# Kernel tuning notes

Measured on AMD Instinct MI355X. Metric: run time of the kernel, lower is better.

The kernel has to match this reference:

```python
import jax, jax.numpy as jnp
import numpy as np

N = 500000
E = 500000
F = 128
BN_EPS = 1e-3


def setup_inputs() -> dict:
    key = jax.random.key(0)
    ks = jax.random.split(key, 8)
    return {
        "x": jax.random.normal(ks[0], (N, F), dtype=jnp.float32),
        "pairs_prev": jax.random.randint(ks[1], (E, 2), 0, N, dtype=jnp.int64),
        "pairs_next": jax.random.randint(ks[2], (E, 2), 0, N, dtype=jnp.int64),
        "w_next": jax.random.normal(ks[3], (F, F), dtype=jnp.float32),
        "w_prev": jax.random.normal(ks[4], (F, F), dtype=jnp.float32),
        "b": jnp.zeros((1, F), dtype=jnp.float32),
        "bn_gamma": jnp.ones((F,), dtype=jnp.float32),
        "bn_beta": jnp.zeros((F,), dtype=jnp.float32),
        "gru_kernel": jax.random.normal(ks[5], (F, 3 * F), dtype=jnp.float32) * 0.1,
        "gru_rec_kernel": jax.random.normal(ks[6], (F, 3 * F), dtype=jnp.float32) * 0.1,
        "gru_bias": jax.random.normal(ks[7], (2, 3 * F), dtype=jnp.float32) * 0.1,
    }


def _gru(x, h, kernel, rec_kernel, bias, hidden):
    matrix_x = x @ kernel + bias[0]            # (N, 3H)
    x_z, x_r, x_h = jnp.split(matrix_x, 3, axis=-1)
    matrix_inner = h @ rec_kernel + bias[1]    # (N, 3H)
    rec_z, rec_r, rec_h = jnp.split(matrix_inner, 3, axis=-1)
    z = jax.nn.sigmoid(x_z + rec_z)
    r = jax.nn.sigmoid(x_r + rec_r)
    h_cand = jnp.tanh(x_h + r * rec_h)
    return z * h + (1.0 - z) * h_cand


def reference(x, pairs_prev, pairs_next, w_next, w_prev, b,
              bn_gamma, bn_beta, gru_kernel, gru_rec_kernel, gru_bias):
    num_nodes = x.shape[0]
    # gather source-node features, scatter-add onto target nodes
    prev_sumx = jax.ops.segment_sum(x[pairs_prev[:, 1]], pairs_prev[:, 0],
                                    num_segments=num_nodes)
    next_sumx = jax.ops.segment_sum(x[pairs_next[:, 1]], pairs_next[:, 0],
                                    num_segments=num_nodes)
    aggre = next_sumx @ w_next + prev_sumx @ w_prev + b
    aggre = aggre + x  # multiply=None -> residual skip
    # BatchNorm1d (training mode): batch mean / biased variance over nodes
    a = jax.nn.relu(aggre)
    mean = jnp.mean(a, axis=0)
    var = jnp.mean((a - mean) ** 2, axis=0)
    a = (a - mean) * jax.lax.rsqrt(var + BN_EPS) * bn_gamma + bn_beta
    return _gru(a, x, gru_kernel, gru_rec_kernel, gru_bias, x.shape[1])
```

## Files before the change

### kernel.cpp

```cpp
#include <hip/hip_runtime.h>
#include <hip/hip_bf16.h>

#define N_NODES 500000
#define E_EDGES 500000
#define FDIM 128
#define BN_EPS 1e-3f
#define OFFS 500001

#define WS_BUCKETS 0
#define WS_SCALESHIFT 16384
#define WS_PW 16640
#define WS_PW2 65792
#define WS_XBF 82176

#define SO_CNT 0
#define SO_OFF 1000000
#define SO_PART 2100000
#define SO_CUR 2200000
#define SO_SRC 3200000

typedef __attribute__((ext_vector_type(4))) float v4f;
typedef __attribute__((ext_vector_type(8))) __bf16 v8bf;

__device__ __forceinline__ unsigned f2bf_u(float f) {
  unsigned u = __float_as_uint(f);
  return ((u + 0x7FFF + ((u >> 16) & 1)) >> 16) & 0xFFFF;
}
__device__ __forceinline__ unsigned f2bf2(float a, float b) {
  return f2bf_u(a) | (f2bf_u(b) << 16);
}
__device__ __forceinline__ float bf2f(unsigned short u) {
  return __uint_as_float((unsigned)u << 16);
}
__device__ __forceinline__ float fast_sigmoid(float x) {
  float e = __expf(-x);
  return __builtin_amdgcn_rcpf(1.f + e);
}
__device__ __forceinline__ float fast_tanh(float x) {
  x = fminf(fmaxf(x, -15.f), 15.f);
  float e = __expf(2.f * x);
  return (e - 1.f) * __builtin_amdgcn_rcpf(e + 1.f);
}

__global__ __launch_bounds__(256) void repack_gru(
    const float* __restrict__ gk, const float* __restrict__ rk,
    unsigned short* __restrict__ pw) {
  int idx = blockIdx.x * 256 + threadIdx.x;
  int side = idx / 49152;
  int rem = idx % 49152;
  int gate = rem >> 14;
  int rr = rem & 16383;
  int c = rr >> 7, k = rr & 127;
  const float* src = side ? rk : gk;
  float v = src[k * 384 + gate * 128 + c];
  int w = c >> 5, nb = (c >> 4) & 1, l15 = c & 15;
  int ks = k >> 5, lg = (k >> 3) & 3, j = k & 7;
  int lane = lg * 16 + l15;
  int e = w * 24576 + ks * 6144 + nb * 3072 + gate * 1024 + side * 512 + lane * 8 + j;
  pw[e] = (unsigned short)f2bf_u(v);
}

__global__ __launch_bounds__(256) void repack_w(
    const float* __restrict__ w_next, const float* __restrict__ w_prev,
    unsigned short* __restrict__ pw2) {
  int idx = blockIdx.x * 256 + threadIdx.x;
  int side = idx >> 14;
  int rr = idx & 16383;
  int c = rr >> 7, k = rr & 127;
  const float* src = side ? w_prev : w_next;
  float v = src[k * 128 + c];
  int nh = c >> 6, nb = (c >> 4) & 3, l15 = c & 15;
  int ks = k >> 5, lg = (k >> 3) & 3, j = k & 7;
  int lane = lg * 16 + l15;
  int e = nh * 16384 + ks * 4096 + nb * 1024 + side * 512 + lane * 8 + j;
  pw2[e] = (unsigned short)f2bf_u(v);
}

__global__ __launch_bounds__(256) void xbf_hist_kernel(
    const float* __restrict__ x, unsigned short* __restrict__ xbf,
    const int* __restrict__ pp, const int* __restrict__ pn,
    unsigned* __restrict__ cnt) {
  size_t i = ((size_t)blockIdx.x * 256 + threadIdx.x) * 8;
  if (i < (size_t)N_NODES * FDIM) {
    float4 a = *(const float4*)(x + i);
    float4 b = *(const float4*)(x + i + 4);
    uint4 o = make_uint4(f2bf2(a.x, a.y), f2bf2(a.z, a.w), f2bf2(b.x, b.y),
                         f2bf2(b.z, b.w));
    *(uint4*)(xbf + i) = o;
  }
  int e = blockIdx.x * 256 + threadIdx.x;
  if (e < 2 * E_EDGES) {
    int side = e >= E_EDGES;
    const int* pair = side ? pn + 2 * (e - E_EDGES) : pp + 2 * e;
    atomicAdd(&cnt[side * N_NODES + pair[0]], 1u);
  }
}

__global__ __launch_bounds__(256) void scan1_kernel(const unsigned* __restrict__ cnt,
                                                    unsigned* __restrict__ off,
                                                    unsigned* __restrict__ part) {
  __shared__ unsigned ls[256];
  int side = blockIdx.y;
  int b = blockIdx.x;
  int td = threadIdx.x;
  int base = b * 1024 + td * 4;
  const unsigned* c = cnt + (size_t)side * N_NODES;
  unsigned v0 = 0, v1 = 0, v2 = 0, v3 = 0;
  if (base + 3 < N_NODES) {
    v0 = c[base]; v1 = c[base + 1]; v2 = c[base + 2]; v3 = c[base + 3];
  } else {
    if (base < N_NODES) v0 = c[base];
    if (base + 1 < N_NODES) v1 = c[base + 1];
    if (base + 2 < N_NODES) v2 = c[base + 2];
  }
  unsigned s = v0 + v1 + v2 + v3;
  ls[td] = s;
  __syncthreads();
  unsigned run = s;
  for (int st = 1; st < 256; st <<= 1) {
    unsigned o = (td >= st) ? ls[td - st] : 0u;
    __syncthreads();
    run += o;
    ls[td] = run;
    __syncthreads();
  }
  unsigned excl = run - s;
  unsigned* oo = off + (size_t)side * OFFS;
  if (base < N_NODES) oo[base] = excl;
  if (base + 1 < N_NODES) oo[base + 1] = excl + v0;
  if (base + 2 < N_NODES) oo[base + 2] = excl + v0 + v1;
  if (base + 3 < N_NODES) oo[base + 3] = excl + v0 + v1 + v2;
  if (td == 255) part[side * 512 + b] = run;
}

__global__ __launch_bounds__(1024) void scan2_kernel(unsigned* __restrict__ part) {
  __shared__ unsigned ls[1024];
  int td = threadIdx.x;
  int b = td & 511;
  unsigned s = part[td];
  ls[td] = s;
  __syncthreads();
  unsigned run = s;
  for (int st = 1; st < 512; st <<= 1) {
    unsigned o = (b >= st) ? ls[td - st] : 0u;
    __syncthreads();
    run += o;
    ls[td] = run;
    __syncthreads();
  }
  part[td] = run - s;
}

__global__ __launch_bounds__(256) void scan3_kernel(unsigned* __restrict__ off,
                                                    const unsigned* __restrict__ part,
                                                    unsigned* __restrict__ cur) {
  int side = blockIdx.y;
  int i = blockIdx.x * 256 + threadIdx.x;
  if (i < N_NODES) {
    unsigned v = off[(size_t)side * OFFS + i] + part[side * 512 + (i >> 10)];
    off[(size_t)side * OFFS + i] = v;
    cur[(size_t)side * N_NODES + i] = v;
  }
  if (i == 0) off[(size_t)side * OFFS + N_NODES] = E_EDGES;
}

__global__ __launch_bounds__(256) void reorder_kernel(const int* __restrict__ pp,
                                                      const int* __restrict__ pn,
                                                      unsigned* __restrict__ cur,
                                                      unsigned* __restrict__ srcbuf) {
  int i = blockIdx.x * 256 + threadIdx.x;
  if (i >= 2 * E_EDGES) return;
  int side = i >= E_EDGES;
  const int* pair = side ? pn + 2 * (i - E_EDGES) : pp + 2 * i;
  unsigned pos = atomicAdd(&cur[(size_t)side * N_NODES + pair[0]], 1u);
  srcbuf[(size_t)side * E_EDGES + pos] = (unsigned)pair[1];
}

__global__ __launch_bounds__(256) void aggre_fused(
    const unsigned short* __restrict__ xbf, const unsigned* __restrict__ off,
    const unsigned* __restrict__ srcbuf, const unsigned short* __restrict__ pw2,
    const float* __restrict__ b, unsigned short* __restrict__ a_out,
    float* __restrict__ buckets) {
  __shared__ unsigned short Ap[32 * 128];
  __shared__ unsigned short An[32 * 128];
  __shared__ unsigned soff[2][33];
  __shared__ float rs[2][128];
  __shared__ float rq[2][128];
  int t = threadIdx.x;
  int r0 = blockIdx.x * 32;
  int rr = t >> 3, fc = t & 7;

  if (t < 33) soff[0][t] = off[r0 + t];
  if (t >= 64 && t < 97) soff[1][t - 64] = off[(size_t)OFFS + r0 + (t - 64)];
  __syncthreads();

#pragma unroll
  for (int side = 0; side < 2; ++side) {
    unsigned s0 = soff[side][rr], s1 = soff[side][rr + 1];
    const unsigned* sl = srcbuf + (size_t)side * E_EDGES;
    float acc[16];
#pragma unroll
    for (int i = 0; i < 16; ++i) acc[i] = 0.f;

    for (unsigned i = s0; i < s1; ++i) {
      size_t s = sl[i];
      const unsigned short* p = xbf + s * FDIM + fc * 16;
      uint4 u0 = *(const uint4*)p;
      uint4 u1 = *(const uint4*)(p + 8);
      acc[0] += bf2f((unsigned short)(u0.x & 0xffff)); acc[1] += __uint_as_float(u0.x & 0xffff0000u);
      acc[2] += bf2f((unsigned short)(u0.y & 0xffff)); acc[3] += __uint_as_float(u0.y & 0xffff0000u);
      acc[4] += bf2f((unsigned short)(u0.z & 0xffff)); acc[5] += __uint_as_float(u0.z & 0xffff0000u);
      acc[6] += bf2f((unsigned short)(u0.w & 0xffff)); acc[7] += __uint_as_float(u0.w & 0xffff0000u);
      acc[8] += bf2f((unsigned short)(u1.x & 0xffff)); acc[9] += __uint_as_float(u1.x & 0xffff0000u);
      acc[10] += bf2f((unsigned short)(u1.y & 0xffff)); acc[11] += __uint_as_float(u1.y & 0xffff0000u);
      acc[12] += bf2f((unsigned short)(u1.z & 0xffff)); acc[13] += __uint_as_float(u1.z & 0xffff0000u);
      acc[14] += bf2f((unsigned short)(u1.w & 0xffff)); acc[15] += __uint_as_float(u1.w & 0xffff0000u);
    }
    unsigned short* dstl = side ? An : Ap;
    int b0 = (rr * 256 + fc * 32) ^ ((rr & 7) << 4);
    int b1 = (rr * 256 + fc * 32 + 16) ^ ((rr & 7) << 4);
    uint4 o0 = make_uint4(f2bf2(acc[0], acc[1]), f2bf2(acc[2], acc[3]),
                          f2bf2(acc[4], acc[5]), f2bf2(acc[6], acc[7]));
    uint4 o1 = make_uint4(f2bf2(acc[8], acc[9]), f2bf2(acc[10], acc[11]),
                          f2bf2(acc[12], acc[13]), f2bf2(acc[14], acc[15]));
    *(uint4*)((char*)dstl + b0) = o0;
    *(uint4*)((char*)dstl + b1) = o1;
  }
  __syncthreads();

  int w = t >> 6, lane = t & 63;
  int m0 = (w & 1) * 16, nh = w >> 1;
  int l15 = lane & 15, lg = lane >> 4;

  v4f acc[4];
#pragma unroll
  for (int nb = 0; nb < 4; ++nb) acc[nb] = (v4f){0.f, 0.f, 0.f, 0.f};

#pragma unroll
  for (int ks = 0; ks < 4; ++ks) {
    int mm = m0 + l15;
    int byte = (mm * 256 + ks * 64 + lg * 16) ^ ((mm & 7) << 4);
    v8bf ap = __builtin_bit_cast(v8bf, *(const uint4*)((const char*)Ap + byte));
    v8bf an = __builtin_bit_cast(v8bf, *(const uint4*)((const char*)An + byte));
    const unsigned short* wb = pw2 + nh * 16384 + ks * 4096 + lane * 8;
#pragma unroll
    for (int nb = 0; nb < 4; ++nb) {
      v8bf bn_ = __builtin_bit_cast(v8bf, *(const uint4*)(wb + nb * 1024));
      v8bf bp_ = __builtin_bit_cast(v8bf, *(const uint4*)(wb + nb * 1024 + 512));
      acc[nb] = __builtin_amdgcn_mfma_f32_16x16x32_bf16(an, bn_, acc[nb], 0, 0, 0);
      acc[nb] = __builtin_amdgcn_mfma_f32_16x16x32_bf16(ap, bp_, acc[nb], 0, 0, 0);
    }
  }

  float s1[4], s2[4];
#pragma unroll
  for (int nb = 0; nb < 4; ++nb) {
    int c = nh * 64 + nb * 16 + l15;
    float bb = b[c];
    s1[nb] = 0.f;
    s2[nb] = 0.f;
#pragma unroll
    for (int r = 0; r < 4; ++r) {
      int row = r0 + m0 + 4 * lg + r;
      size_t o = (size_t)row * FDIM + c;
      float v = acc[nb][r] + bb + bf2f(xbf[o]);
      v = fmaxf(v, 0.f);
      a_out[o] = (unsigned short)f2bf_u(v);
      s1[nb] += v;
      s2[nb] += v * v;
    }
    s1[nb] += __shfl_xor(s1[nb], 16);
    s1[nb] += __shfl_xor(s1[nb], 32);
    s2[nb] += __shfl_xor(s2[nb], 16);
    s2[nb] += __shfl_xor(s2[nb], 32);
  }
  if (lane < 16) {
#pragma unroll
    for (int nb = 0; nb < 4; ++nb) {
      rs[w & 1][nh * 64 + nb * 16 + lane] = s1[nb];
      rq[w & 1][nh * 64 + nb * 16 + lane] = s2[nb];
    }
  }
  __syncthreads();
  if (t < 128) {
    float s = rs[0][t] + rs[1][t];
    float q = rq[0][t] + rq[1][t];
    float* bkt = buckets + (size_t)(blockIdx.x & 63) * 256;
    atomicAdd(bkt + t, s);
    atomicAdd(bkt + 128 + t, q);
  }
}

__global__ void bn_finalize(const float* __restrict__ buckets,
                            const float* __restrict__ gamma,
                            const float* __restrict__ beta,
                            float* __restrict__ scaleshift) {
  int t = threadIdx.x;
  float s = 0.f, q = 0.f;
  for (int j = 0; j < 64; ++j) {
    s += buckets[j * 256 + t];
    q += buckets[j * 256 + 128 + t];
  }
  float mean = s / (float)N_NODES;
  float var = q / (float)N_NODES - mean * mean;
  var = fmaxf(var, 0.f);
  float sc = gamma[t] * rsqrtf(var + BN_EPS);
  scaleshift[t] = sc;
  scaleshift[128 + t] = beta[t] - mean * sc;
}

__global__ __launch_bounds__(256) void gru_mfma(
    const unsigned short* __restrict__ a_bf, const unsigned short* __restrict__ xbf,
    const unsigned short* __restrict__ pw, const float* __restrict__ gbias,
    const float* __restrict__ scaleshift, float* __restrict__ out) {
  __shared__ unsigned short Aa[32 * 128];
  __shared__ unsigned short Ax[32 * 128];
  int t = threadIdx.x;
  int r0 = blockIdx.x * 32;

#pragma unroll
  for (int i = 0; i < 2; ++i) {
    int q = t + 256 * i;
    int row = q >> 4, kq = q & 15;
    size_t g = (size_t)(r0 + row) * FDIM + kq * 8;
    uint4 av = *(const uint4*)(a_bf + g);
    uint4 xv = *(const uint4*)(xbf + g);
    float4 sc0 = *(const float4*)(scaleshift + kq * 8);
    float4 sc1 = *(const float4*)(scaleshift + kq * 8 + 4);
    float4 sh0 = *(const float4*)(scaleshift + 128 + kq * 8);
    float4 sh1 = *(const float4*)(scaleshift + 128 + kq * 8 + 4);
    float a0 = __uint_as_float(av.x << 16), a1 = __uint_as_float(av.x & 0xffff0000u);
    float a2 = __uint_as_float(av.y << 16), a3 = __uint_as_float(av.y & 0xffff0000u);
    float a4 = __uint_as_float(av.z << 16), a5 = __uint_as_float(av.z & 0xffff0000u);
    float a6 = __uint_as_float(av.w << 16), a7 = __uint_as_float(av.w & 0xffff0000u);
    uint4 na = make_uint4(f2bf2(a0 * sc0.x + sh0.x, a1 * sc0.y + sh0.y),
                          f2bf2(a2 * sc0.z + sh0.z, a3 * sc0.w + sh0.w),
                          f2bf2(a4 * sc1.x + sh1.x, a5 * sc1.y + sh1.y),
                          f2bf2(a6 * sc1.z + sh1.z, a7 * sc1.w + sh1.w));
    int byte = (row * 256 + kq * 16) ^ ((row & 7) << 4);
    *(uint4*)((char*)Aa + byte) = na;
    *(uint4*)((char*)Ax + byte) = xv;
  }
  __syncthreads();

  int w = t >> 6, lane = t & 63;
  int l15 = lane & 15, lg = lane >> 4;

  v4f az[2][2], ar[2][2], ah0[2][2], ah1[2][2];
#pragma unroll
  for (int m = 0; m < 2; ++m)
#pragma unroll
    for (int nb = 0; nb < 2; ++nb) {
      az[m][nb] = (v4f){0.f, 0.f, 0.f, 0.f};
      ar[m][nb] = (v4f){0.f, 0.f, 0.f, 0.f};
      ah0[m][nb] = (v4f){0.f, 0.f, 0.f, 0.f};
      ah1[m][nb] = (v4f){0.f, 0.f, 0.f, 0.f};
    }

#pragma unroll
  for (int ks = 0; ks < 4; ++ks) {
    v8bf aa[2], ax[2];
#pragma unroll
    for (int m = 0; m < 2; ++m) {
      int mm = m * 16 + l15;
      int byte = (mm * 256 + ks * 64 + lg * 16) ^ ((mm & 7) << 4);
      aa[m] = __builtin_bit_cast(v8bf, *(const uint4*)((const char*)Aa + byte));
      ax[m] = __builtin_bit_cast(v8bf, *(const uint4*)((const char*)Ax + byte));
    }
    const unsigned short* wb = pw + w * 24576 + ks * 6144 + lane * 8;
#pragma unroll
    for (int nb = 0; nb < 2; ++nb) {
      const unsigned short* wn = wb + nb * 3072;
      v8bf b0z = __builtin_bit_cast(v8bf, *(const uint4*)(wn));
      v8bf b1z = __builtin_bit_cast(v8bf, *(const uint4*)(wn + 512));
      v8bf b0r = __builtin_bit_cast(v8bf, *(const uint4*)(wn + 1024));
      v8bf b1r = __builtin_bit_cast(v8bf, *(const uint4*)(wn + 1536));
      v8bf b0h = __builtin_bit_cast(v8bf, *(const uint4*)(wn + 2048));
      v8bf b1h = __builtin_bit_cast(v8bf, *(const uint4*)(wn + 2560));
#pragma unroll
      for (int m = 0; m < 2; ++m) {
        az[m][nb] = __builtin_amdgcn_mfma_f32_16x16x32_bf16(aa[m], b0z, az[m][nb], 0, 0, 0);
        az[m][nb] = __builtin_amdgcn_mfma_f32_16x16x32_bf16(ax[m], b1z, az[m][nb], 0, 0, 0);
        ar[m][nb] = __builtin_amdgcn_mfma_f32_16x16x32_bf16(aa[m], b0r, ar[m][nb], 0, 0, 0);
        ar[m][nb] = __builtin_amdgcn_mfma_f32_16x16x32_bf16(ax[m], b1r, ar[m][nb], 0, 0, 0);
        ah0[m][nb] = __builtin_amdgcn_mfma_f32_16x16x32_bf16(aa[m], b0h, ah0[m][nb], 0, 0, 0);
        ah1[m][nb] = __builtin_amdgcn_mfma_f32_16x16x32_bf16(ax[m], b1h, ah1[m][nb], 0, 0, 0);
      }
    }
  }

#pragma unroll
  for (int nb = 0; nb < 2; ++nb) {
    int c = w * 32 + nb * 16 + l15;
    float bz = gbias[c] + gbias[384 + c];
    float br = gbias[128 + c] + gbias[512 + c];
    float bh0 = gbias[256 + c];
    float bh1 = gbias[640 + c];
#pragma unroll
    for (int m = 0; m < 2; ++m) {
#pragma unroll
      for (int r = 0; r < 4; ++r) {
        int rl = m * 16 + 4 * lg + r;
        int row = r0 + rl;
        float z = fast_sigmoid(az[m][nb][r] + bz);
        float rg = fast_sigmoid(ar[m][nb][r] + br);
        float hc = fast_tanh(ah0[m][nb][r] + bh0 + rg * (ah1[m][nb][r] + bh1));
        int hb = (rl * 256 + c * 2) ^ ((rl & 7) << 4);
        float h = bf2f(*(const unsigned short*)((const char*)Ax + hb));
        __builtin_nontemporal_store(z * h + (1.f - z) * hc,
                                    out + (size_t)row * FDIM + c);
      }
    }
  }
}

extern "C" void kernel_launch(void* const* d_in, const int* in_sizes, int n_in,
                              void* d_out, int out_size, void* d_ws, size_t ws_size,
                              hipStream_t stream) {
  const float* x = (const float*)d_in[0];
  const int* pp = (const int*)d_in[1];
  const int* pn = (const int*)d_in[2];
  const float* w_next = (const float*)d_in[3];
  const float* w_prev = (const float*)d_in[4];
  const float* b = (const float*)d_in[5];
  const float* gamma = (const float*)d_in[6];
  const float* beta = (const float*)d_in[7];
  const float* gk = (const float*)d_in[8];
  const float* rk = (const float*)d_in[9];
  const float* gbias = (const float*)d_in[10];
  float* out = (float*)d_out;
  float* ws = (float*)d_ws;

  float* buckets = ws + WS_BUCKETS;
  float* scaleshift = ws + WS_SCALESHIFT;
  unsigned short* pw = (unsigned short*)(ws + WS_PW);
  unsigned short* pw2 = (unsigned short*)(ws + WS_PW2);
  unsigned short* xbf = (unsigned short*)(ws + WS_XBF);
  unsigned short* a_bf = xbf + (size_t)N_NODES * FDIM;

  unsigned* u = (unsigned*)d_out;
  unsigned* cnt = u + SO_CNT;
  unsigned* off = u + SO_OFF;
  unsigned* part = u + SO_PART;
  unsigned* cur = u + SO_CUR;
  unsigned* srcbuf = u + SO_SRC;

  hipMemsetAsync(cnt, 0, 2u * N_NODES * sizeof(unsigned), stream);
  hipMemsetAsync(part, 0, 1024 * sizeof(unsigned), stream);
  hipMemsetAsync(buckets, 0, (16384 + 256) * sizeof(float), stream);

  repack_gru<<<384, 256, 0, stream>>>(gk, rk, pw);
  repack_w<<<128, 256, 0, stream>>>(w_next, w_prev, pw2);
  xbf_hist_kernel<<<31250, 256, 0, stream>>>(x, xbf, pp, pn, cnt);

  scan1_kernel<<<dim3(489, 2), 256, 0, stream>>>(cnt, off, part);
  scan2_kernel<<<1, 1024, 0, stream>>>(part);
  scan3_kernel<<<dim3((N_NODES + 255) / 256, 2), 256, 0, stream>>>(off, part, cur);
  reorder_kernel<<<(2 * E_EDGES + 255) / 256, 256, 0, stream>>>(pp, pn, cur, srcbuf);

  aggre_fused<<<N_NODES / 32, 256, 0, stream>>>(xbf, off, srcbuf, pw2, b, a_bf,
                                                buckets);
  bn_finalize<<<1, 128, 0, stream>>>(buckets, gamma, beta, scaleshift);
  gru_mfma<<<N_NODES / 32, 256, 0, stream>>>(a_bf, xbf, pw, gbias, scaleshift, out);
}
```

Before: 509.1 us.

## Fold BatchNorm scale and shift into GRU input kernel weights and bias

The per-channel BatchNorm scale is now multiplied into the GRU input-kernel rows during repacking, and the shift is folded into a precomputed bias vector by a small single-block kernel. The GRU kernel then stages the raw activations into shared memory without a per-element affine transform and bf16 re-rounding. Weight repacking moves after bn_finalize, which adds two small dependent launches to the critical path. It also changes where bf16 rounding happens, since scaled weights are rounded instead of normalized activations.

Measured after the change: 507.4 us. Within noise of the previous version (-0.3%).

```diff
diff --git a/kernel.cpp b/kernel.cpp
--- a/kernel.cpp
+++ b/kernel.cpp
@@ -42,9 +42,9 @@
   return (e - 1.f) * __builtin_amdgcn_rcpf(e + 1.f);
 }
 
-__global__ __launch_bounds__(256) void repack_gru(
+__global__ __launch_bounds__(256) void repack_gru_scaled(
     const float* __restrict__ gk, const float* __restrict__ rk,
-    unsigned short* __restrict__ pw) {
+    const float* __restrict__ scaleshift, unsigned short* __restrict__ pw) {
   int idx = blockIdx.x * 256 + threadIdx.x;
   int side = idx / 49152;
   int rem = idx % 49152;
@@ -53,11 +53,31 @@
   int c = rr >> 7, k = rr & 127;
   const float* src = side ? rk : gk;
   float v = src[k * 384 + gate * 128 + c];
+  if (side == 0) v *= scaleshift[k];
   int w = c >> 5, nb = (c >> 4) & 1, l15 = c & 15;
   int ks = k >> 5, lg = (k >> 3) & 3, j = k & 7;
   int lane = lg * 16 + l15;
   int e = w * 24576 + ks * 6144 + nb * 3072 + gate * 1024 + side * 512 + lane * 8 + j;
   pw[e] = (unsigned short)f2bf_u(v);
+}
+
+__global__ __launch_bounds__(512) void bias_fold(
+    const float* __restrict__ gk, const float* __restrict__ gbias,
+    const float* __restrict__ scaleshift, float* __restrict__ gbias2) {
+  __shared__ float sh[128];
+  int j = threadIdx.x;
+  if (j < 128) sh[j] = scaleshift[128 + j];
+  __syncthreads();
+  if (j < 384) {
+    float s = 0.f;
+#pragma unroll 8
+    for (int k = 0; k < 128; ++k) s += sh[k] * gk[k * 384 + j];
+    float o = gbias[j] + s;
+    if (j < 256) o += gbias[384 + j];
+    gbias2[j] = o;
+  } else {
+    gbias2[j] = gbias[256 + j];
+  }
 }
 
 __global__ __launch_bounds__(256) void repack_w(
@@ -311,8 +331,8 @@
 
 __global__ __launch_bounds__(256) void gru_mfma(
     const unsigned short* __restrict__ a_bf, const unsigned short* __restrict__ xbf,
-    const unsigned short* __restrict__ pw, const float* __restrict__ gbias,
-    const float* __restrict__ scaleshift, float* __restrict__ out) {
+    const unsigned short* __restrict__ pw, const float* __restrict__ gbias2,
+    float* __restrict__ out) {
   __shared__ unsigned short Aa[32 * 128];
   __shared__ unsigned short Ax[32 * 128];
   int t = threadIdx.x;
@@ -325,20 +345,8 @@
     size_t g = (size_t)(r0 + row) * FDIM + kq * 8;
     uint4 av = *(const uint4*)(a_bf + g);
     uint4 xv = *(const uint4*)(xbf + g);
-    float4 sc0 = *(const float4*)(scaleshift + kq * 8);
-    float4 sc1 = *(const float4*)(scaleshift + kq * 8 + 4);
-    float4 sh0 = *(const float4*)(scaleshift + 128 + kq * 8);
-    float4 sh1 = *(const float4*)(scaleshift + 128 + kq * 8 + 4);
-    float a0 = __uint_as_float(av.x << 16), a1 = __uint_as_float(av.x & 0xffff0000u);
-    float a2 = __uint_as_float(av.y << 16), a3 = __uint_as_float(av.y & 0xffff0000u);
-    float a4 = __uint_as_float(av.z << 16), a5 = __uint_as_float(av.z & 0xffff0000u);
-    float a6 = __uint_as_float(av.w << 16), a7 = __uint_as_float(av.w & 0xffff0000u);
-    uint4 na = make_uint4(f2bf2(a0 * sc0.x + sh0.x, a1 * sc0.y + sh0.y),
-                          f2bf2(a2 * sc0.z + sh0.z, a3 * sc0.w + sh0.w),
-                          f2bf2(a4 * sc1.x + sh1.x, a5 * sc1.y + sh1.y),
-                          f2bf2(a6 * sc1.z + sh1.z, a7 * sc1.w + sh1.w));
     int byte = (row * 256 + kq * 16) ^ ((row & 7) << 4);
-    *(uint4*)((char*)Aa + byte) = na;
+    *(uint4*)((char*)Aa + byte) = av;
     *(uint4*)((char*)Ax + byte) = xv;
   }
   __syncthreads();
@@ -392,10 +400,10 @@
 #pragma unroll
   for (int nb = 0; nb < 2; ++nb) {
     int c = w * 32 + nb * 16 + l15;
-    float bz = gbias[c] + gbias[384 + c];
-    float br = gbias[128 + c] + gbias[512 + c];
-    float bh0 = gbias[256 + c];
-    float bh1 = gbias[640 + c];
+    float bz = gbias2[c];
+    float br = gbias2[128 + c];
+    float bh0 = gbias2[256 + c];
+    float bh1 = gbias2[384 + c];
 #pragma unroll
     for (int m = 0; m < 2; ++m) {
 #pragma unroll
@@ -432,6 +440,7 @@
   float* ws = (float*)d_ws;
 
   float* buckets = ws + WS_BUCKETS;
+  float* gbias2 = ws + WS_BUCKETS;
   float* scaleshift = ws + WS_SCALESHIFT;
   unsigned short* pw = (unsigned short*)(ws + WS_PW);
   unsigned short* pw2 = (unsigned short*)(ws + WS_PW2);
@@ -449,7 +458,6 @@
   hipMemsetAsync(part, 0, 1024 * sizeof(unsigned), stream);
   hipMemsetAsync(buckets, 0, (16384 + 256) * sizeof(float), stream);
 
-  repack_gru<<<384, 256, 0, stream>>>(gk, rk, pw);
   repack_w<<<128, 256, 0, stream>>>(w_next, w_prev, pw2);
   xbf_hist_kernel<<<31250, 256, 0, stream>>>(x, xbf, pp, pn, cnt);
 
@@ -461,5 +469,7 @@
   aggre_fused<<<N_NODES / 32, 256, 0, stream>>>(xbf, off, srcbuf, pw2, b, a_bf,
                                                 buckets);
   bn_finalize<<<1, 128, 0, stream>>>(buckets, gamma, beta, scaleshift);
-  gru_mfma<<<N_NODES / 32, 256, 0, stream>>>(a_bf, xbf, pw, gbias, scaleshift, out);
-}
+  repack_gru_scaled<<<384, 256, 0, stream>>>(gk, rk, scaleshift, pw);
+  bias_fold<<<1, 512, 0, stream>>>(gk, gbias, scaleshift, gbias2);
+  gru_mfma<<<N_NODES / 32, 256, 0, stream>>>(a_bf, xbf, pw, gbias2, out);
+}
```
